# Kernel tuning notes

Hardware: AMD Instinct MI355X
Metric: run time of the kernel (lower is better)

Reference implementation:

```python
import jax, jax.numpy as jnp
import numpy as np

N_NODES = 50000


def setup_inputs() -> dict:
    key = jax.random.key(0)
    ks = jax.random.split(key, 8)
    d_in, d_h, d_out = 128, 128, 1
    s_in = 1.0 / np.sqrt(d_in)
    s_h = 1.0 / np.sqrt(d_h)
    return {
        "x": jax.random.normal(ks[0], (N_NODES, d_in), dtype=jnp.float32),
        "edge_index": jax.random.randint(ks[1], (2, 800000), 0, N_NODES, dtype=jnp.int64),
        "W1a": jax.random.normal(ks[2], (d_in, d_h), dtype=jnp.float32) * s_in,
        "b1a": jnp.zeros((d_h,), dtype=jnp.float32),
        "W1b": jax.random.normal(ks[3], (d_h, d_h), dtype=jnp.float32) * s_h,
        "b1b": jnp.zeros((d_h,), dtype=jnp.float32),
        "W2a": jax.random.normal(ks[4], (d_h, d_h), dtype=jnp.float32) * s_h,
        "b2a": jnp.zeros((d_h,), dtype=jnp.float32),
        "W2b": jax.random.normal(ks[5], (d_h, d_h), dtype=jnp.float32) * s_h,
        "b2b": jnp.zeros((d_h,), dtype=jnp.float32),
        "Wfc": jax.random.normal(ks[6], (d_h, d_out), dtype=jnp.float32) * s_h,
        "bfc": jnp.zeros((d_out,), dtype=jnp.float32),
    }


def _gin_conv(x, src, dst, Wa, ba, Wb, bb):
    # GINConv (eps=0): h_i = MLP((1+eps)*x_i + sum_{j->i} x_j)
    agg = jax.ops.segment_sum(x[src], dst, num_segments=N_NODES)
    h = x + agg
    h = jax.nn.relu(h @ Wa + ba)
    h = jax.nn.relu(h @ Wb + bb)
    return h


def reference(x, edge_index, W1a, b1a, W1b, b1b, W2a, b2a, W2b, b2b, Wfc, bfc):
    src, dst = edge_index[0], edge_index[1]
    h = _gin_conv(x, src, dst, W1a, b1a, W1b, b1b)
    h = _gin_conv(h, src, dst, W2a, b2a, W2b, b2b)
    out = h @ Wfc + bfc
    return jax.nn.sigmoid(out)
```

## Files before the change

### kernel.cpp

```cpp
#include <hip/hip_runtime.h>
#include <hip/hip_fp16.h>
#include <cstdint>
#include <cstddef>

#define D 128
#define NP 8
#define S_CSR 48
typedef __attribute__((ext_vector_type(8))) _Float16 half8;
typedef __attribute__((ext_vector_type(4))) float f32x4;
typedef __attribute__((ext_vector_type(4))) uint uint4n;

__device__ __forceinline__ uint pack2h(float x, float y) {
    __half2 h = __floats2half2_rn(x, y);
    return *(uint*)&h;
}
__device__ __forceinline__ __half2 u2h(uint u) { return *(__half2*)&u; }
__device__ __forceinline__ uint h2u(__half2 h) { return *(uint*)&h; }
__device__ __forceinline__ int pad16(int v) { return (v + 15) & ~15; }

__global__ __launch_bounds__(256) void prep(const float* __restrict__ x,
                                            uint* __restrict__ X32,
                                            const float* __restrict__ W0,
                                            const float* __restrict__ W1,
                                            const float* __restrict__ W2,
                                            const float* __restrict__ W3,
                                            ushort* __restrict__ P0,
                                            ushort* __restrict__ P1,
                                            ushort* __restrict__ P2,
                                            ushort* __restrict__ P3,
                                            int* __restrict__ cnt,
                                            uint* __restrict__ zrow0,
                                            uint* __restrict__ zrow2,
                                            ushort* __restrict__ csr,
                                            int M, int cvtB, int mB) {
    int b = blockIdx.x, t = threadIdx.x;
    if (b < cvtB) {
        long long gid = (long long)b * 256 + t;
        if (gid >= (long long)M * 16) return;
        int node = (int)(gid >> 4), q = (int)(gid & 15);
        const f32x4* xp = (const f32x4*)(x + (size_t)node * D + q * 8);
        f32x4 v0 = __builtin_nontemporal_load(xp);
        f32x4 v1 = __builtin_nontemporal_load(xp + 1);
        uint4n o;
        o.x = pack2h(v0.x, v0.y); o.y = pack2h(v0.z, v0.w);
        o.z = pack2h(v1.x, v1.y); o.w = pack2h(v1.z, v1.w);
        ((uint4n*)X32)[(size_t)node * 16 + q] = o;
    } else if (b < cvtB + 256) {
        int o = ((b - cvtB) & 63) * 256 + t;
        int which = (b - cvtB) >> 6;
        const float* W = which == 0 ? W0 : which == 1 ? W1 : which == 2 ? W2 : W3;
        ushort* P = which == 0 ? P0 : which == 1 ? P1 : which == 2 ? P2 : P3;
        int j = o & 7, g = (o >> 3) & 3, n = (o >> 5) & 127, ks = o >> 12;
        int k = ks * 32 + g * 8 + j;
        __half h = __float2half_rn(W[k * 128 + n]);
        P[o] = *(ushort*)&h;
    } else if (b < cvtB + 256 + mB) {
        int i = (b - cvtB - 256) * 256 + t;
        if (i < M) cnt[i] = 0;
        if (b == cvtB + 256 && t < 64) {
            zrow0[(size_t)M * 64 + t] = 0u;
            zrow2[(size_t)M * 64 + t] = 0u;
        }
    } else {
        long long idx = (long long)(b - cvtB - 256 - mB) * 256 + t;
        long long tot = (long long)M * (S_CSR / 2);
        uint sv = (uint)M | ((uint)M << 16);
        if (idx < tot) ((uint*)csr)[idx] = sv;
    }
}

__global__ __launch_bounds__(256) void fill_csr_part(const int* __restrict__ ei,
                                                     int* __restrict__ cnt,
                                                     ushort* __restrict__ csr,
                                                     int E, int M, int nslice) {
    int p = blockIdx.x & (NP - 1);
    int slice = blockIdx.x >> 3;
    int psz = (M + NP - 1) / NP;
    int lo = p * psz, hi = min(M, lo + psz);
    int eps = (E + nslice - 1) / nslice;
    int e0 = slice * eps, e1 = min(E, e0 + eps);
    const unsigned int* eu = (const unsigned int*)ei;
    int sh = (eu[1] == 0u && eu[3] == 0u && eu[5] == 0u && eu[7] == 0u) ? 1 : 0;
    const int* sp = ei;
    const int* dp = sp + ((long long)E << sh);
#pragma unroll 4
    for (int e = e0 + threadIdx.x; e < e1; e += 256) {
        int d = __builtin_nontemporal_load(dp + ((long long)e << sh));
        if (d >= lo && d < hi) {
            int s = __builtin_nontemporal_load(sp + ((long long)e << sh));
            int pos = atomicAdd(&cnt[d], 1);
            if (pos < S_CSR) csr[(size_t)d * S_CSR + pos] = (ushort)s;
        }
    }
}

__global__ __launch_bounds__(256) void aggregate_f16(const uint* __restrict__ X,
                                                     const int* __restrict__ cnt,
                                                     const ushort* __restrict__ csr,
                                                     uint* __restrict__ H, int M) {
    int wv = __builtin_amdgcn_readfirstlane((int)(threadIdx.x >> 6));
    int node = blockIdx.x * 4 + wv;
    if (node >= M) return;
    int lane = threadIdx.x & 63;

    int degp = min(pad16(__builtin_amdgcn_readfirstlane(cnt[node])), S_CSR);
    const ushort* ep = csr + (size_t)node * S_CSR;

    __half2 acc = u2h(X[(size_t)node * 64 + lane]);
    for (int j0 = 0; j0 < degp; j0 += 16) {
        uint4n i0 = *(const uint4n*)(ep + j0);
        uint4n i1 = *(const uint4n*)(ep + j0 + 8);
        uint us[16];
        us[0]  = X[(size_t)(i0.x & 0xffff) * 64 + lane];
        us[1]  = X[(size_t)(i0.x >> 16)    * 64 + lane];
        us[2]  = X[(size_t)(i0.y & 0xffff) * 64 + lane];
        us[3]  = X[(size_t)(i0.y >> 16)    * 64 + lane];
        us[4]  = X[(size_t)(i0.z & 0xffff) * 64 + lane];
        us[5]  = X[(size_t)(i0.z >> 16)    * 64 + lane];
        us[6]  = X[(size_t)(i0.w & 0xffff) * 64 + lane];
        us[7]  = X[(size_t)(i0.w >> 16)    * 64 + lane];
        us[8]  = X[(size_t)(i1.x & 0xffff) * 64 + lane];
        us[9]  = X[(size_t)(i1.x >> 16)    * 64 + lane];
        us[10] = X[(size_t)(i1.y & 0xffff) * 64 + lane];
        us[11] = X[(size_t)(i1.y >> 16)    * 64 + lane];
        us[12] = X[(size_t)(i1.z & 0xffff) * 64 + lane];
        us[13] = X[(size_t)(i1.z >> 16)    * 64 + lane];
        us[14] = X[(size_t)(i1.w & 0xffff) * 64 + lane];
        us[15] = X[(size_t)(i1.w >> 16)    * 64 + lane];
        __half2 t0 = __hadd2(__hadd2(u2h(us[0]), u2h(us[1])), __hadd2(u2h(us[2]), u2h(us[3])));
        __half2 t1 = __hadd2(__hadd2(u2h(us[4]), u2h(us[5])), __hadd2(u2h(us[6]), u2h(us[7])));
        __half2 t2 = __hadd2(__hadd2(u2h(us[8]), u2h(us[9])), __hadd2(u2h(us[10]), u2h(us[11])));
        __half2 t3 = __hadd2(__hadd2(u2h(us[12]), u2h(us[13])), __hadd2(u2h(us[14]), u2h(us[15])));
        acc = __hadd2(acc, __hadd2(__hadd2(t0, t1), __hadd2(t2, t3)));
    }
    __builtin_nontemporal_store(h2u(acc), &H[(size_t)node * 64 + lane]);
}

template <int FINAL>
__global__ __launch_bounds__(256) void mlp_mfma(const ushort* __restrict__ A,
                                                const ushort* __restrict__ Bpa,
                                                const float* __restrict__ ba,
                                                const ushort* __restrict__ Bpb,
                                                const float* __restrict__ bb,
                                                const float* __restrict__ Wfc,
                                                const float* __restrict__ bfc,
                                                ushort* __restrict__ C,
                                                float* __restrict__ out,
                                                int M, int nTiles) {
    __shared__ ushort sB[2][16384];
    __shared__ ushort Hs[4][16][16][8];
    int t = threadIdx.x;
    int wv = t >> 6, lane = t & 63;
    int l15 = lane & 15, g = lane >> 4;

    for (int i = t; i < 2048; i += 256) {
        ((uint4n*)sB[0])[i] = ((const uint4n*)Bpa)[i];
        ((uint4n*)sB[1])[i] = ((const uint4n*)Bpb)[i];
    }
    __syncthreads();

    float bva[8], bvb[8], wf[8];
#pragma unroll
    for (int nt = 0; nt < 8; ++nt) {
        bva[nt] = ba[nt * 16 + l15];
        bvb[nt] = bb[nt * 16 + l15];
        if (FINAL) wf[nt] = Wfc[nt * 16 + l15];
    }
    float bf = FINAL ? bfc[0] : 0.f;

    for (int tile = blockIdx.x; tile < nTiles; tile += gridDim.x) {
        int rb = tile * 64 + wv * 16;
        int arow = rb + l15;
        int arow_c = arow < M ? arow : M - 1;

        half8 a_frag[4];
        const uint4n* ap = (const uint4n*)(A + (size_t)arow_c * D + g * 8);
#pragma unroll
        for (int ks = 0; ks < 4; ++ks) {
            uint4n u = __builtin_nontemporal_load(ap + ks * 4);
            a_frag[ks] = *(half8*)&u;
        }

        f32x4 acc[8];
#pragma unroll
        for (int i = 0; i < 8; ++i) acc[i] = (f32x4){0.f, 0.f, 0.f, 0.f};
#pragma unroll
        for (int ks = 0; ks < 4; ++ks) {
#pragma unroll
            for (int nt = 0; nt < 8; ++nt) {
                half8 b = *(const half8*)&sB[0][((ks * 128 + nt * 16 + l15) * 4 + g) << 3];
                acc[nt] = __builtin_amdgcn_mfma_f32_16x16x32_f16(a_frag[ks], b, acc[nt], 0, 0, 0);
            }
        }
#pragma unroll
        for (int nt = 0; nt < 8; ++nt) {
            int col = nt * 16 + l15;
            int u = col >> 3, j = col & 7;
#pragma unroll
            for (int r = 0; r < 4; ++r) {
                int row = g * 4 + r;
                float v = fmaxf(acc[nt][r] + bva[nt], 0.f);
                __half hh = __float2half_rn(v);
                Hs[wv][row][u ^ row][j] = *(ushort*)&hh;
            }
        }

        f32x4 acc2[8];
#pragma unroll
        for (int i = 0; i < 8; ++i) acc2[i] = (f32x4){0.f, 0.f, 0.f, 0.f};
#pragma unroll
        for (int ks = 0; ks < 4; ++ks) {
            half8 a = *(const half8*)&Hs[wv][l15][(ks * 4 + g) ^ l15][0];
#pragma unroll
            for (int nt = 0; nt < 8; ++nt) {
                half8 b = *(const half8*)&sB[1][((ks * 128 + nt * 16 + l15) * 4 + g) << 3];
                acc2[nt] = __builtin_amdgcn_mfma_f32_16x16x32_f16(a, b, acc2[nt], 0, 0, 0);
            }
        }

        if (!FINAL) {
#pragma unroll
            for (int nt = 0; nt < 8; ++nt) {
                int col = nt * 16 + l15;
#pragma unroll
                for (int r = 0; r < 4; ++r) {
                    int row = rb + g * 4 + r;
                    if (row < M) {
                        float v = fmaxf(acc2[nt][r] + bvb[nt], 0.f);
                        __half hh = __float2half_rn(v);
                        C[(size_t)row * D + col] = *(ushort*)&hh;
                    }
                }
            }
        } else {
            float p[4] = {0.f, 0.f, 0.f, 0.f};
#pragma unroll
            for (int nt = 0; nt < 8; ++nt) {
#pragma unroll
                for (int r = 0; r < 4; ++r) {
                    float v = fmaxf(acc2[nt][r] + bvb[nt], 0.f);
                    p[r] = fmaf(v, wf[nt], p[r]);
                }
            }
#pragma unroll
            for (int r = 0; r < 4; ++r) {
                p[r] += __shfl_xor(p[r], 1);
                p[r] += __shfl_xor(p[r], 2);
                p[r] += __shfl_xor(p[r], 4);
                p[r] += __shfl_xor(p[r], 8);
            }
            if (l15 == 0) {
#pragma unroll
                for (int r = 0; r < 4; ++r) {
                    int row = rb + g * 4 + r;
                    if (row < M) out[row] = 1.f / (1.f + expf(-(p[r] + bf)));
                }
            }
        }
    }
}

extern "C" void kernel_launch(void* const* d_in, const int* in_sizes, int n_in,
                              void* d_out, int out_size, void* d_ws, size_t ws_size,
                              hipStream_t stream) {
    const float* x   = (const float*)d_in[0];
    const void*  ei  = d_in[1];
    const float* W1a = (const float*)d_in[2];
    const float* b1a = (const float*)d_in[3];
    const float* W1b = (const float*)d_in[4];
    const float* b1b = (const float*)d_in[5];
    const float* W2a = (const float*)d_in[6];
    const float* b2a = (const float*)d_in[7];
    const float* W2b = (const float*)d_in[8];
    const float* b2b = (const float*)d_in[9];
    const float* Wfc = (const float*)d_in[10];
    const float* bfc = (const float*)d_in[11];
    float* out = (float*)d_out;

    int M = in_sizes[0] / D;
    int E = in_sizes[1] / 2;
    size_t nf2 = (size_t)(M + 1) * D;

    ushort* B0 = (ushort*)d_ws;
    ushort* B1 = B0 + nf2;
    ushort* B2 = B1 + nf2;
    ushort* P1a = B2 + nf2;
    ushort* P1b = P1a + 16384;
    ushort* P2a = P1b + 16384;
    ushort* P2b = P2a + 16384;
    int* cnt    = (int*)(P2b + 16384);
    ushort* csr = (ushort*)(cnt + M);

    int mBlocks = (M + 255) / 256;
    int cvtB = (M * 16 + 255) / 256;
    int csrB = (int)(((long long)M * (S_CSR / 2) + 255) / 256);
    int aggBlocks = (M + 3) / 4;
    int nTiles = (M + 63) / 64;
    int nslice = 256;

    prep<<<cvtB + 256 + mBlocks + csrB, 256, 0, stream>>>(
        x, (uint*)B0, W1a, W1b, W2a, W2b, P1a, P1b, P2a, P2b,
        cnt, (uint*)B0, (uint*)B2, csr, M, cvtB, mBlocks);

    fill_csr_part<<<NP * nslice, 256, 0, stream>>>((const int*)ei, cnt, csr, E, M, nslice);

    aggregate_f16<<<aggBlocks, 256, 0, stream>>>((const uint*)B0, cnt, csr, (uint*)B1, M);
    mlp_mfma<0><<<512, 256, 0, stream>>>(B1, P1a, b1a, P1b, b1b, nullptr, nullptr, B2, nullptr, M, nTiles);

    aggregate_f16<<<aggBlocks, 256, 0, stream>>>((const uint*)B2, cnt, csr, (uint*)B0, M);
    mlp_mfma<1><<<512, 256, 0, stream>>>(B0, P2a, b2a, P2b, b2b, Wfc, bfc, nullptr, out, M, nTiles);
}
```

Measured before the change: 144.1 us.

## Split CSR init into own kernel and overlap CSR fill with input conversion

```diff
diff --git a/kernel.cpp b/kernel.cpp
--- a/kernel.cpp
+++ b/kernel.cpp
@@ -6,6 +6,7 @@
 #define D 128
 #define NP 8
 #define S_CSR 48
+#define NSLICE 128
 typedef __attribute__((ext_vector_type(8))) _Float16 half8;
 typedef __attribute__((ext_vector_type(4))) float f32x4;
 typedef __attribute__((ext_vector_type(4))) uint uint4n;
@@ -18,7 +19,31 @@
 __device__ __forceinline__ uint h2u(__half2 h) { return *(uint*)&h; }
 __device__ __forceinline__ int pad16(int v) { return (v + 15) & ~15; }
 
-__global__ __launch_bounds__(256) void prep(const float* __restrict__ x,
+__global__ __launch_bounds__(256) void init_csr(int* __restrict__ cnt,
+                                                ushort* __restrict__ csr,
+                                                uint* __restrict__ zrow0,
+                                                uint* __restrict__ zrow2,
+                                                int M, int csrB) {
+    int b = blockIdx.x, t = threadIdx.x;
+    if (b < csrB) {
+        long long idx = (long long)b * 256 + t;
+        long long tot = (long long)M * (S_CSR / 2);
+        uint sv = (uint)M | ((uint)M << 16);
+        if (idx < tot) ((uint*)csr)[idx] = sv;
+    } else {
+        int i = (b - csrB) * 256 + t;
+        if (i < M) cnt[i] = 0;
+        if (b == csrB && t < 64) {
+            zrow0[(size_t)M * 64 + t] = 0u;
+            zrow2[(size_t)M * 64 + t] = 0u;
+        }
+    }
+}
+
+__global__ __launch_bounds__(256) void mega(const int* __restrict__ ei,
+                                            int* __restrict__ cnt,
+                                            ushort* __restrict__ csr,
+                                            const float* __restrict__ x,
                                             uint* __restrict__ X32,
                                             const float* __restrict__ W0,
                                             const float* __restrict__ W1,
@@ -28,14 +53,30 @@
                                             ushort* __restrict__ P1,
                                             ushort* __restrict__ P2,
                                             ushort* __restrict__ P3,
-                                            int* __restrict__ cnt,
-                                            uint* __restrict__ zrow0,
-                                            uint* __restrict__ zrow2,
-                                            ushort* __restrict__ csr,
-                                            int M, int cvtB, int mB) {
+                                            int E, int M, int cvtB) {
     int b = blockIdx.x, t = threadIdx.x;
-    if (b < cvtB) {
-        long long gid = (long long)b * 256 + t;
+    if (b < NP * NSLICE) {
+        int p = b & (NP - 1);
+        int slice = b >> 3;
+        int psz = (M + NP - 1) / NP;
+        int lo = p * psz, hi = min(M, lo + psz);
+        int eps = (E + NSLICE - 1) / NSLICE;
+        int e0 = slice * eps, e1 = min(E, e0 + eps);
+        const unsigned int* eu = (const unsigned int*)ei;
+        int sh = (eu[1] == 0u && eu[3] == 0u && eu[5] == 0u && eu[7] == 0u) ? 1 : 0;
+        const int* sp = ei;
+        const int* dp = sp + ((long long)E << sh);
+#pragma unroll 8
+        for (int e = e0 + t; e < e1; e += 256) {
+            int d = dp[(long long)e << sh];
+            if (d >= lo && d < hi) {
+                int s = sp[(long long)e << sh];
+                int pos = atomicAdd(&cnt[d], 1);
+                if (pos < S_CSR) csr[(size_t)d * S_CSR + pos] = (ushort)s;
+            }
+        }
+    } else if (b < NP * NSLICE + cvtB) {
+        long long gid = (long long)(b - NP * NSLICE) * 256 + t;
         if (gid >= (long long)M * 16) return;
         int node = (int)(gid >> 4), q = (int)(gid & 15);
         const f32x4* xp = (const f32x4*)(x + (size_t)node * D + q * 8);
@@ -45,52 +86,16 @@
         o.x = pack2h(v0.x, v0.y); o.y = pack2h(v0.z, v0.w);
         o.z = pack2h(v1.x, v1.y); o.w = pack2h(v1.z, v1.w);
         ((uint4n*)X32)[(size_t)node * 16 + q] = o;
-    } else if (b < cvtB + 256) {
-        int o = ((b - cvtB) & 63) * 256 + t;
-        int which = (b - cvtB) >> 6;
+    } else {
+        int rb = b - NP * NSLICE - cvtB;
+        int o = (rb & 63) * 256 + t;
+        int which = rb >> 6;
         const float* W = which == 0 ? W0 : which == 1 ? W1 : which == 2 ? W2 : W3;
         ushort* P = which == 0 ? P0 : which == 1 ? P1 : which == 2 ? P2 : P3;
         int j = o & 7, g = (o >> 3) & 3, n = (o >> 5) & 127, ks = o >> 12;
         int k = ks * 32 + g * 8 + j;
         __half h = __float2half_rn(W[k * 128 + n]);
         P[o] = *(ushort*)&h;
-    } else if (b < cvtB + 256 + mB) {
-        int i = (b - cvtB - 256) * 256 + t;
-        if (i < M) cnt[i] = 0;
-        if (b == cvtB + 256 && t < 64) {
-            zrow0[(size_t)M * 64 + t] = 0u;
-            zrow2[(size_t)M * 64 + t] = 0u;
-        }
-    } else {
-        long long idx = (long long)(b - cvtB - 256 - mB) * 256 + t;
-        long long tot = (long long)M * (S_CSR / 2);
-        uint sv = (uint)M | ((uint)M << 16);
-        if (idx < tot) ((uint*)csr)[idx] = sv;
-    }
-}
-
-__global__ __launch_bounds__(256) void fill_csr_part(const int* __restrict__ ei,
-                                                     int* __restrict__ cnt,
-                                                     ushort* __restrict__ csr,
-                                                     int E, int M, int nslice) {
-    int p = blockIdx.x & (NP - 1);
-    int slice = blockIdx.x >> 3;
-    int psz = (M + NP - 1) / NP;
-    int lo = p * psz, hi = min(M, lo + psz);
-    int eps = (E + nslice - 1) / nslice;
-    int e0 = slice * eps, e1 = min(E, e0 + eps);
-    const unsigned int* eu = (const unsigned int*)ei;
-    int sh = (eu[1] == 0u && eu[3] == 0u && eu[5] == 0u && eu[7] == 0u) ? 1 : 0;
-    const int* sp = ei;
-    const int* dp = sp + ((long long)E << sh);
-#pragma unroll 4
-    for (int e = e0 + threadIdx.x; e < e1; e += 256) {
-        int d = __builtin_nontemporal_load(dp + ((long long)e << sh));
-        if (d >= lo && d < hi) {
-            int s = __builtin_nontemporal_load(sp + ((long long)e << sh));
-            int pos = atomicAdd(&cnt[d], 1);
-            if (pos < S_CSR) csr[(size_t)d * S_CSR + pos] = (ushort)s;
-        }
     }
 }
 
@@ -296,13 +301,12 @@
     int csrB = (int)(((long long)M * (S_CSR / 2) + 255) / 256);
     int aggBlocks = (M + 3) / 4;
     int nTiles = (M + 63) / 64;
-    int nslice = 256;
-
-    prep<<<cvtB + 256 + mBlocks + csrB, 256, 0, stream>>>(
-        x, (uint*)B0, W1a, W1b, W2a, W2b, P1a, P1b, P2a, P2b,
-        cnt, (uint*)B0, (uint*)B2, csr, M, cvtB, mBlocks);
-
-    fill_csr_part<<<NP * nslice, 256, 0, stream>>>((const int*)ei, cnt, csr, E, M, nslice);
+
+    init_csr<<<csrB + mBlocks, 256, 0, stream>>>(cnt, csr, (uint*)B0, (uint*)B2, M, csrB);
+
+    mega<<<NP * NSLICE + cvtB + 256, 256, 0, stream>>>(
+        (const int*)ei, cnt, csr, x, (uint*)B0,
+        W1a, W1b, W2a, W2b, P1a, P1b, P2a, P2b, E, M, cvtB);
 
     aggregate_f16<<<aggBlocks, 256, 0, stream>>>((const uint*)B0, cnt, csr, (uint*)B1, M);
     mlp_mfma<0><<<512, 256, 0, stream>>>(B1, P1a, b1a, P1b, b1b, nullptr, nullptr, B2, nullptr, M, nTiles);
```

After: 143.9 us. Within noise of the previous version (-0.1%).
